# Kernel optimization log

Measured on AMD Instinct MI355X. Metric: run time of the kernel, lower is better.

## Reference

```python
import jax, jax.numpy as jnp
import numpy as np
from jax import lax

EPS = 1e-5
F_CH = 32  # TIM future channels = int(256/8)
B_CH = 32  # TIM past channels (note: source bug -> these are zeroed, not shifted)


def inorm(x):
    # InstanceNorm3d (no affine): normalize each (b, c) over (T, H, W), biased var
    m = jnp.mean(x, axis=(2, 3, 4), keepdims=True)
    v = jnp.var(x, axis=(2, 3, 4), keepdims=True)
    return (x - m) * lax.rsqrt(v + EPS)


def conv1x1(x, w):
    # pointwise conv: x [B,C,T,H,W], w [O,C]
    return jnp.einsum('bcthw,oc->bothw', x, w)


def dwconv(x, w, pad):
    # depthwise 3D conv; w [C,1,kd,kh,kw], pad = [(pd,pd),(ph,ph),(pw,pw)]
    return lax.conv_general_dilated(
        x, w, window_strides=(1, 1, 1), padding=pad,
        feature_group_count=x.shape[1],
        dimension_numbers=('NCDHW', 'OIDHW', 'NCDHW'))


def tim(x):
    # Non-circular temporal interlacing. Faithful to source (past slice is a no-op):
    # channels [0:f]  <- x shifted from future (t+1), zero-padded at last frame
    # channels [f:f+b] <- zeros
    # channels [f+b:] <- identity
    f, b = F_CH, B_CH
    fut = jnp.concatenate([x[:, :f, 1:], jnp.zeros_like(x[:, :f, :1])], axis=2)
    mid = jnp.zeros_like(x[:, f:f + b])
    return jnp.concatenate([fut, mid, x[:, f + b:]], axis=1)


def setup_inputs() -> dict:
    key = jax.random.key(0)
    ks = jax.random.split(key, 7)
    cin, hid, cout = 64, 256, 64
    x = jax.random.normal(ks[0], (4, cin, 16, 64, 64), dtype=jnp.float32)
    w1 = jax.random.normal(ks[1], (hid, cin), dtype=jnp.float32) * 0.05
    w_dw_s = jax.random.normal(ks[2], (hid, 1, 1, 3, 3), dtype=jnp.float32) * 0.1
    w_dw_t = jax.random.normal(ks[3], (hid, 1, 3, 1, 1), dtype=jnp.float32) * 0.1
    w_se1 = jax.random.normal(ks[4], (hid // 4, hid), dtype=jnp.float32) * 0.05
    w_se2 = jax.random.normal(ks[5], (hid, hid // 4), dtype=jnp.float32) * 0.05
    w_proj = jax.random.normal(ks[6], (cout, hid), dtype=jnp.float32) * 0.05
    return {'x': x, 'w1': w1, 'w_dw_s': w_dw_s, 'w_dw_t': w_dw_t,
            'w_se1': w_se1, 'w_se2': w_se2, 'w_proj': w_proj}


def reference(x, w1, w_dw_s, w_dw_t, w_se1, w_se2, w_proj):
    shortcut = x
    # stage1: expand 1x1 conv + IN + ReLU
    h = jax.nn.relu(inorm(conv1x1(x, w1)))
    # temporal interlace (zero-FLOP channel shift)
    h = tim(h)
    # stage2: depthwise spatial (1,3,3) + IN + ReLU
    h = jax.nn.relu(inorm(dwconv(h, w_dw_s, [(0, 0), (1, 1), (1, 1)])))
    # stage3: depthwise temporal (3,1,1) + IN + ReLU
    h = jax.nn.relu(inorm(dwconv(h, w_dw_t, [(1, 1), (0, 0), (0, 0)])))
    # squeeze-excite
    y = jnp.mean(h, axis=(2, 3, 4), keepdims=True)           # [B,C,1,1,1]
    y = jax.nn.relu(jnp.einsum('bcthw,oc->bothw', y, w_se1))
    y = jax.nn.sigmoid(jnp.einsum('bcthw,oc->bothw', y, w_se2))
    h = h * y
    # proj 1x1 + IN, residual, maxpool (1,2,2)
    out = inorm(conv1x1(h, w_proj)) + shortcut
    out = lax.reduce_window(out, -jnp.inf, lax.max,
                            (1, 1, 1, 2, 2), (1, 1, 1, 2, 2), 'VALID')
    return out
```

## Files before the change

kernel.cpp:

```cpp
#include <hip/hip_runtime.h>
#include <hip/hip_bf16.h>

#define B_   4
#define CIN  64
#define HID  256
#define COUT 64
#define T_   16
#define H_   64
#define W_   64
#define HW_  (H_*W_)
#define THW  (T_*HW_)
#define EPS  1e-5f

typedef unsigned short ushort_t;
typedef unsigned int   uint_t;
typedef short bf16x8 __attribute__((ext_vector_type(8)));
typedef float f32x4  __attribute__((ext_vector_type(4)));

#define SM3   4096
#define SIS3  5120
#define SSES  6144
#define SAL   7168
#define SBE   8192
__device__ float g_stats[10240];
__device__ float g_eps [4*1024*256];
__device__ float g_epss[4*1024*256];
__device__ ushort_t g_wpack[32768];

__device__ __forceinline__ float bf2f(ushort_t u) {
    return __uint_as_float(((uint_t)u) << 16);
}
__device__ __forceinline__ ushort_t f2bf(float f) {
    uint_t u = __float_as_uint(f);
    uint_t r = u + 0x7fffu + ((u >> 16) & 1u);
    return (ushort_t)(r >> 16);
}
__device__ __forceinline__ void loadnorm8(const ushort_t* p, float a, float bb,
                                          float* v) {
    uint4 u = *(const uint4*)p;
    uint_t uu[4] = {u.x, u.y, u.z, u.w};
    #pragma unroll
    for (int j = 0; j < 4; ++j) {
        v[2*j]   = fmaxf(fmaf(__uint_as_float(uu[j] << 16),         a, bb), 0.f);
        v[2*j+1] = fmaxf(fmaf(__uint_as_float(uu[j] & 0xffff0000u), a, bb), 0.f);
    }
}
__device__ __forceinline__ void loadnorm4(const ushort_t* p, float a, float bb,
                                          float* v) {
    uint2 u = *(const uint2*)p;
    uint_t uu[2] = {u.x, u.y};
    #pragma unroll
    for (int j = 0; j < 2; ++j) {
        v[2*j]   = fmaxf(fmaf(__uint_as_float(uu[j] << 16),         a, bb), 0.f);
        v[2*j+1] = fmaxf(fmaf(__uint_as_float(uu[j] & 0xffff0000u), a, bb), 0.f);
    }
}
__device__ __forceinline__ void unpacknorm2(uint2 k, float a, float bb, float* v) {
    uint_t uu[2] = {k.x, k.y};
    #pragma unroll
    for (int j = 0; j < 2; ++j) {
        v[2*j]   = fmaxf(fmaf(__uint_as_float(uu[j] << 16),         a, bb), 0.f);
        v[2*j+1] = fmaxf(fmaf(__uint_as_float(uu[j] & 0xffff0000u), a, bb), 0.f);
    }
}

__global__ __launch_bounds__(256) void k_prep(const float* __restrict__ w1,
                                              const float* __restrict__ wproj) {
    int idx = blockIdx.x*256 + threadIdx.x;
    {
        int j = idx & 7, lane = (idx>>3) & 63, ot = (idx>>9) & 3;
        int ks = (idx>>11) & 1, wv = idx >> 12;
        int ln = lane & 15, q = lane >> 4;
        int o = wv*64 + ot*16 + ln, k = ks*32 + q*8 + j;
        g_wpack[idx] = f2bf(w1[o*CIN + k]);
    }
    {
        int j = idx & 7, lane = (idx>>3) & 63, ot = (idx>>9) & 3, kg = idx >> 11;
        int ln = lane & 15, q = lane >> 4;
        int o = ot*16 + ln, k = kg*32 + q*8 + j;
        g_wpack[16384 + idx] = f2bf(wproj[o*HID + k]);
    }
}

__global__ __launch_bounds__(256) void k_expand(const float* __restrict__ x,
                                                ushort_t* __restrict__ h1, int b0) {
    union SMem {
        ushort_t Bs[64*72];
        float    red[2][256][16];
    };
    __shared__ SMem sm;
    const int tid = threadIdx.x;
    const int bb  = blockIdx.y, gb = b0 + bb;
    const int pos0 = blockIdx.x * 64;
    const int lane = tid & 63, wv = tid >> 6;
    const int q = lane >> 4, ln = lane & 15;

    bf16x8 af[2][4];
    #pragma unroll
    for (int ks = 0; ks < 2; ++ks)
        #pragma unroll
        for (int ot = 0; ot < 4; ++ot)
            af[ks][ot] = *(const bf16x8*)&g_wpack[(((wv*2+ks)*4+ot)<<9) + lane*8];

    #pragma unroll
    for (int i = 0; i < 4; ++i) {
        int lin = i*1024 + tid*4;
        int k = lin >> 6, n0 = lin & 63;
        float4 v = *(const float4*)&x[(size_t)(gb*CIN + k) * THW + pos0 + n0];
        ushort_t* d = &sm.Bs[k*72 + ((n0 + 16*((k>>3)&3)) & 63)];
        d[0] = f2bf(v.x); d[1] = f2bf(v.y); d[2] = f2bf(v.z); d[3] = f2bf(v.w);
    }
    __syncthreads();

    f32x4 acc[4][4];
    #pragma unroll
    for (int i = 0; i < 4; ++i)
        #pragma unroll
        for (int j = 0; j < 4; ++j)
            acc[i][j] = (f32x4){0.f,0.f,0.f,0.f};

    #pragma unroll
    for (int ks = 0; ks < 2; ++ks) {
        bf16x8 bfr[4];
        #pragma unroll
        for (int nt = 0; nt < 4; ++nt) {
            union { short s[8]; bf16x8 v; } bu;
            #pragma unroll
            for (int j = 0; j < 8; ++j) {
                int k = ks*32 + q*8 + j;
                int nn = (nt*16 + ln + 16*((k>>3)&3)) & 63;
                bu.s[j] = (short)sm.Bs[k*72 + nn];
            }
            bfr[nt] = bu.v;
        }
        #pragma unroll
        for (int ot = 0; ot < 4; ++ot)
            #pragma unroll
            for (int nt = 0; nt < 4; ++nt)
                acc[ot][nt] = __builtin_amdgcn_mfma_f32_16x16x32_bf16(
                    af[ks][ot], bfr[nt], acc[ot][nt], 0, 0, 0);
    }

    float sp_[16], ssp_[16];
    #pragma unroll
    for (int i = 0; i < 16; ++i) { sp_[i] = 0.f; ssp_[i] = 0.f; }

    #pragma unroll
    for (int ot = 0; ot < 4; ++ot)
        #pragma unroll
        for (int nt = 0; nt < 4; ++nt)
            #pragma unroll
            for (int r = 0; r < 4; ++r) {
                float vv = acc[ot][nt][r];
                int o = wv*64 + ot*16 + q*4 + r;
                int n = nt*16 + ln;
                h1[((size_t)bb*HID + o)*THW + pos0 + n] = f2bf(vv);
                sp_[ot*4+r] += vv;
                ssp_[ot*4+r] = fmaf(vv, vv, ssp_[ot*4+r]);
            }

    __syncthreads();
    #pragma unroll
    for (int i = 0; i < 16; ++i) {
        int o = wv*64 + (i>>2)*16 + q*4 + (i&3);
        sm.red[0][o][ln] = sp_[i];
        sm.red[1][o][ln] = ssp_[i];
    }
    __syncthreads();
    {
        float s = 0.f, ss = 0.f;
        #pragma unroll
        for (int l = 0; l < 16; ++l) {
            s  += sm.red[0][tid][l];
            ss += sm.red[1][tid][l];
        }
        size_t base = ((size_t)bb*1024 + blockIdx.x)*256 + tid;
        g_eps [base] = s;
        g_epss[base] = ss;
    }
}

__global__ __launch_bounds__(1024) void k_mid(const ushort_t* __restrict__ h1,
                                              const float* __restrict__ wdws,
                                              const float* __restrict__ wdwt,
                                              ushort_t* __restrict__ h3) {
    const int tid = threadIdx.x;
    const int bc  = blockIdx.x;
    const int o   = bc & (HID-1);
    const int bb  = bc >> 8;
    const int wid = tid >> 6, lane = tid & 63;

    if (o >= 32 && o < 64) {
        if (tid == 0) {
            g_stats[SM3  + bc] = 0.f;
            g_stats[SIS3 + bc] = 1.f / sqrtf(EPS);
            g_stats[SSES + bc] = 0.f;
        }
        return;
    }

    __shared__ float pl[2][64*65];
    __shared__ float ls[16], lss[16];
    __shared__ float sa, sb;

    {
        const float* ps  = &g_eps [((size_t)bb*1024)*256 + o];
        const float* pss = &g_epss[((size_t)bb*1024)*256 + o];
        float s  = ps [(size_t)tid*256];
        float ss = pss[(size_t)tid*256];
        #pragma unroll
        for (int m = 32; m > 0; m >>= 1) {
            s  += __shfl_xor(s,  m);
            ss += __shfl_xor(ss, m);
        }
        if (lane == 0) { ls[wid] = s; lss[wid] = ss; }
        __syncthreads();
        if (tid == 0) {
            float st = 0.f, sst = 0.f;
            #pragma unroll
            for (int i = 0; i < 16; ++i) { st += ls[i]; sst += lss[i]; }
            float m = st * (1.f/THW);
            float v = sst * (1.f/THW) - m*m;
            float is = 1.f / sqrtf(v + EPS);
            sa = is; sb = -m * is;
        }
        __syncthreads();
    }
    const float a1 = sa, b1 = sb;

    const int fut = (o < 32) ? 1 : 0;
    const int y   = tid >> 4;
    const int x0  = (tid & 15) * 4;
    const ushort_t* chp = h1 + (size_t)bc * THW;

    float wf[9];
    #pragma unroll
    for (int k = 0; k < 9; ++k) wf[k] = wdws[o*9 + k];

    {
        const ushort_t* sp = chp + (size_t)(fut ? 1 : 0) * HW_ + tid*4;
        float v[4];
        loadnorm4(sp, a1, b1, v);
        float* dst = &pl[0][y*65 + x0];
        #pragma unroll
        for (int i = 0; i < 4; ++i) dst[i] = v[i];
    }
    __syncthreads();

    uint2 keep[16];
    float s2 = 0.f, ss2 = 0.f;
    const int lastp = fut ? (T_-2) : (T_-1);

    #pragma unroll
    for (int t = 0; t < T_; ++t) {
        if (t < lastp) {
            int np = t + 1;
            const ushort_t* sp = chp + (size_t)(fut ? np+1 : np)*HW_ + tid*4;
            float v[4];
            loadnorm4(sp, a1, b1, v);
            float* dst = &pl[np & 1][y*65 + x0];
            #pragma unroll
            for (int i = 0; i < 4; ++i) dst[i] = v[i];
        }
        if (fut && t == T_-1) {
            keep[t] = (uint2){0u, 0u};
        } else {
            const float* plane = pl[t & 1];
            float v[3][6];
            #pragma unroll
            for (int dy = 0; dy < 3; ++dy) {
                int yy = y + dy - 1;
                if (yy < 0 || yy >= H_) {
                    #pragma unroll
                    for (int j = 0; j < 6; ++j) v[dy][j] = 0.f;
                } else {
                    const float* rp = &plane[yy*65];
                    v[dy][0] = (x0 == 0)  ? 0.f : rp[x0-1];
                    #pragma unroll
                    for (int i = 0; i < 4; ++i) v[dy][1+i] = rp[x0+i];
                    v[dy][5] = (x0 == 60) ? 0.f : rp[x0+4];
                }
            }
            uint_t outp[2];
            #pragma unroll
            for (int i2 = 0; i2 < 2; ++i2) {
                float o0 = 0.f, o1 = 0.f;
                #pragma unroll
                for (int dy = 0; dy < 3; ++dy)
                    #pragma unroll
                    for (int dx = 0; dx < 3; ++dx) {
                        float w = wf[dy*3+dx];
                        o0 = fmaf(w, v[dy][2*i2 + dx],     o0);
                        o1 = fmaf(w, v[dy][2*i2 + 1 + dx], o1);
                    }
                ushort_t u0 = f2bf(o0), u1 = f2bf(o1);
                float r0 = bf2f(u0), r1 = bf2f(u1);
                s2 += r0 + r1; ss2 = fmaf(r0, r0, fmaf(r1, r1, ss2));
                outp[i2] = (uint_t)u0 | ((uint_t)u1 << 16);
            }
            keep[t].x = outp[0]; keep[t].y = outp[1];
        }
        __syncthreads();
    }

    {
        float s = s2, ss = ss2;
        #pragma unroll
        for (int m = 32; m > 0; m >>= 1) {
            s  += __shfl_xor(s,  m);
            ss += __shfl_xor(ss, m);
        }
        if (lane == 0) { ls[wid] = s; lss[wid] = ss; }
        __syncthreads();
        if (tid == 0) {
            float st = 0.f, sst = 0.f;
            #pragma unroll
            for (int i = 0; i < 16; ++i) { st += ls[i]; sst += lss[i]; }
            float m = st * (1.f/THW);
            float v = sst * (1.f/THW) - m*m;
            float is = 1.f / sqrtf(v + EPS);
            sa = is; sb = -m * is;
        }
        __syncthreads();
    }
    const float a2 = sa, b2 = sb;

    const float w0 = wdwt[o*3+0], w1 = wdwt[o*3+1], w2 = wdwt[o*3+2];
    ushort_t* op = h3 + (size_t)bc * THW + tid*4;

    float p[4], c[4], n[4];
    #pragma unroll
    for (int i = 0; i < 4; ++i) p[i] = 0.f;
    unpacknorm2(keep[0], a2, b2, c);
    unpacknorm2(keep[1], a2, b2, n);

    float s3 = 0.f, ss3 = 0.f;
    #pragma unroll
    for (int t = 0; t < T_; ++t) {
        uint_t outp[2];
        #pragma unroll
        for (int i2 = 0; i2 < 2; ++i2) {
            float o0 = fmaf(w0, p[2*i2],   fmaf(w1, c[2*i2],   w2 * n[2*i2]));
            float o1 = fmaf(w0, p[2*i2+1], fmaf(w1, c[2*i2+1], w2 * n[2*i2+1]));
            ushort_t u0 = f2bf(o0), u1 = f2bf(o1);
            float r0 = bf2f(u0), r1 = bf2f(u1);
            s3 += r0 + r1; ss3 = fmaf(r0, r0, fmaf(r1, r1, ss3));
            outp[i2] = (uint_t)u0 | ((uint_t)u1 << 16);
        }
        uint2 r; r.x = outp[0]; r.y = outp[1];
        *(uint2*)(op + (size_t)t*HW_) = r;

        #pragma unroll
        for (int i = 0; i < 4; ++i) { p[i] = c[i]; c[i] = n[i]; }
        if (t + 2 < T_) unpacknorm2(keep[t+2], a2, b2, n);
        else {
            #pragma unroll
            for (int i = 0; i < 4; ++i) n[i] = 0.f;
        }
        keep[t] = r;
    }

    {
        float s = s3, ss = ss3;
        #pragma unroll
        for (int m = 32; m > 0; m >>= 1) {
            s  += __shfl_xor(s,  m);
            ss += __shfl_xor(ss, m);
        }
        if (lane == 0) { ls[wid] = s; lss[wid] = ss; }
        __syncthreads();
        if (tid == 0) {
            float st = 0.f, sst = 0.f;
            #pragma unroll
            for (int i = 0; i < 16; ++i) { st += ls[i]; sst += lss[i]; }
            float m = st * (1.f/THW);
            float v = sst * (1.f/THW) - m*m;
            float is = 1.f / sqrtf(v + EPS);
            g_stats[SM3  + bc] = m;
            g_stats[SIS3 + bc] = is;
            sa = is; sb = -m * is;
        }
        __syncthreads();
    }

    const float a3 = sa, b3 = sb;
    float sse = 0.f;
    #pragma unroll
    for (int t = 0; t < T_; ++t) {
        uint_t uu[2] = {keep[t].x, keep[t].y};
        #pragma unroll
        for (int j = 0; j < 2; ++j) {
            sse += fmaxf(fmaf(__uint_as_float(uu[j] << 16),         a3, b3), 0.f);
            sse += fmaxf(fmaf(__uint_as_float(uu[j] & 0xffff0000u), a3, b3), 0.f);
        }
    }
    #pragma unroll
    for (int m = 32; m > 0; m >>= 1) sse += __shfl_xor(sse, m);
    if (lane == 0) ls[wid] = sse;
    __syncthreads();
    if (tid == 0) {
        float st = 0.f;
        #pragma unroll
        for (int i = 0; i < 16; ++i) st += ls[i];
        g_stats[SSES + bc] = st * (1.f/THW);
    }
}

__global__ __launch_bounds__(256) void k_semlp(const float* __restrict__ wse1,
                                               const float* __restrict__ wse2) {
    __shared__ float mv[HID];
    __shared__ float y1[64];
    const int bb = blockIdx.x, tid = threadIdx.x;
    mv[tid] = g_stats[SSES + bb*HID + tid];
    __syncthreads();
    if (tid < 64) {
        float acc = 0.f;
        #pragma unroll 8
        for (int c = 0; c < HID; ++c) acc = fmaf(wse1[tid*HID + c], mv[c], acc);
        y1[tid] = fmaxf(acc, 0.f);
    }
    __syncthreads();
    float z = 0.f;
    #pragma unroll
    for (int c = 0; c < 64; ++c) z = fmaf(wse2[tid*64 + c], y1[c], z);
    float se = 1.f / (1.f + expf(-z));
    const int bc = bb*HID + tid;
    float al = g_stats[SIS3 + bc] * se;
    if (tid >= 32 && tid < 64) al = 0.f;
    g_stats[SAL + bc] = al;
    g_stats[SBE + bc] = -g_stats[SM3 + bc] * al;
}

__global__ __launch_bounds__(256) void k_proj(const ushort_t* __restrict__ h3,
                                              float* __restrict__ proj) {
    __shared__ ushort_t Bs[64*136];
    const int tid = threadIdx.x;
    const int bb  = blockIdx.y;
    const int pos0 = blockIdx.x * 128;
    const int lane = tid & 63, wv = tid >> 6;
    const int q = lane >> 4, ln = lane & 15;

    f32x4 acc[4][2];
    #pragma unroll
    for (int i = 0; i < 4; ++i) {
        acc[i][0] = (f32x4){0.f,0.f,0.f,0.f};
        acc[i][1] = (f32x4){0.f,0.f,0.f,0.f};
    }

    for (int kc = 0; kc < 4; ++kc) {
        #pragma unroll
        for (int i = 0; i < 8; ++i) {
            int lin = i*1024 + tid*4;
            int kl = lin >> 7, n0 = lin & 127;
            int ch = bb*HID + kc*64 + kl;
            float al = g_stats[SAL + ch], be = g_stats[SBE + ch];
            ushort_t* d = &Bs[kl*136 + ((n0 + 16*((kl>>3)&7)) & 127)];
            if (al == 0.f) {
                d[0] = 0; d[1] = 0; d[2] = 0; d[3] = 0;
            } else {
                uint2 u = *(const uint2*)&h3[(size_t)ch * THW + pos0 + n0];
                float f0 = __uint_as_float(u.x << 16);
                float f1 = __uint_as_float(u.x & 0xffff0000u);
                float f2 = __uint_as_float(u.y << 16);
                float f3 = __uint_as_float(u.y & 0xffff0000u);
                d[0] = f2bf(fmaxf(fmaf(f0, al, be), 0.f));
                d[1] = f2bf(fmaxf(fmaf(f1, al, be), 0.f));
                d[2] = f2bf(fmaxf(fmaf(f2, al, be), 0.f));
                d[3] = f2bf(fmaxf(fmaf(f3, al, be), 0.f));
            }
        }
        __syncthreads();

        #pragma unroll
        for (int ks = 0; ks < 2; ++ks) {
            int kg = kc*2 + ks;
            bf16x8 af[4];
            #pragma unroll
            for (int ot = 0; ot < 4; ++ot)
                af[ot] = *(const bf16x8*)&g_wpack[16384 + ((kg*4+ot)<<9) + lane*8];
            bf16x8 bfr[2];
            #pragma unroll
            for (int nt = 0; nt < 2; ++nt) {
                union { short s[8]; bf16x8 v; } bu;
                #pragma unroll
                for (int j = 0; j < 8; ++j) {
                    int kl = ks*32 + q*8 + j;
                    int nn = (wv*32 + nt*16 + ln + 16*((kl>>3)&7)) & 127;
                    bu.s[j] = (short)Bs[kl*136 + nn];
                }
                bfr[nt] = bu.v;
            }
            #pragma unroll
            for (int ot = 0; ot < 4; ++ot)
                #pragma unroll
                for (int nt = 0; nt < 2; ++nt)
                    acc[ot][nt] = __builtin_amdgcn_mfma_f32_16x16x32_bf16(
                        af[ot], bfr[nt], acc[ot][nt], 0, 0, 0);
        }
        __syncthreads();
    }

    #pragma unroll
    for (int ot = 0; ot < 4; ++ot)
        #pragma unroll
        for (int nt = 0; nt < 2; ++nt)
            #pragma unroll
            for (int r = 0; r < 4; ++r) {
                int o = ot*16 + q*4 + r;
                int n = wv*32 + nt*16 + ln;
                proj[((size_t)bb*COUT + o)*THW + pos0 + n] = acc[ot][nt][r];
            }
}

__global__ __launch_bounds__(1024) void k_final(const float* __restrict__ proj,
                                                const float* __restrict__ x,
                                                float* __restrict__ out, int b0) {
    const int bo  = blockIdx.x;
    const int tid = threadIdx.x;
    const float* p = proj + (size_t)bo * THW;

    float s = 0.f, ss = 0.f;
    #pragma unroll
    for (int i = 0; i < THW/(1024*4); ++i) {
        float4 u = *(const float4*)(p + i*4096 + tid*4);
        s += u.x; ss = fmaf(u.x, u.x, ss);
        s += u.y; ss = fmaf(u.y, u.y, ss);
        s += u.z; ss = fmaf(u.z, u.z, ss);
        s += u.w; ss = fmaf(u.w, u.w, ss);
    }
    #pragma unroll
    for (int off = 32; off > 0; off >>= 1) {
        s  += __shfl_down(s,  off, 64);
        ss += __shfl_down(ss, off, 64);
    }
    __shared__ float ls[16], lss[16];
    __shared__ float sa, sb;
    int wid = tid >> 6, lane = tid & 63;
    if (lane == 0) { ls[wid] = s; lss[wid] = ss; }
    __syncthreads();
    if (tid == 0) {
        float st = 0.f, sst = 0.f;
        #pragma unroll
        for (int i = 0; i < 16; ++i) { st += ls[i]; sst += lss[i]; }
        float m = st * (1.f/THW);
        float v = sst * (1.f/THW) - m*m;
        float is = 1.f / sqrtf(v + EPS);
        sa = is; sb = -m * is;
    }
    __syncthreads();
    const float a = sa, bb = sb;

    const size_t gbase = (size_t)(b0*COUT + bo) * THW;
    float* op = out + (size_t)(b0*COUT + bo) * (T_*1024);
    #pragma unroll
    for (int i = 0; i < 16; ++i) {
        int idx = i*1024 + tid;
        int xx = idx & 31, yy = (idx >> 5) & 31, t = idx >> 10;
        float m = -3.4e38f;
        #pragma unroll
        for (int r = 0; r < 2; ++r) {
            size_t off = (size_t)t*HW_ + (size_t)(2*yy + r)*W_ + 2*xx;
            float2 p2 = *(const float2*)(p + off);
            float2 x2 = *(const float2*)(x + gbase + off);
            float v0 = fmaf(p2.x, a, bb) + x2.x;
            float v1 = fmaf(p2.y, a, bb) + x2.y;
            m = fmaxf(m, fmaxf(v0, v1));
        }
        op[idx] = m;
    }
}

extern "C" void kernel_launch(void* const* d_in, const int* in_sizes, int n_in,
                              void* d_out, int out_size, void* d_ws, size_t ws_size,
                              hipStream_t stream) {
    const float* x     = (const float*)d_in[0];
    const float* w1    = (const float*)d_in[1];
    const float* wdws  = (const float*)d_in[2];
    const float* wdwt  = (const float*)d_in[3];
    const float* wse1  = (const float*)d_in[4];
    const float* wse2  = (const float*)d_in[5];
    const float* wproj = (const float*)d_in[6];
    float* out = (float*)d_out;

    const size_t perb = 2ull * HID * THW * sizeof(ushort_t);
    int nb = (ws_size >= 4*perb) ? 4 : (ws_size >= 2*perb) ? 2 : 1;

    k_prep<<<64, 256, 0, stream>>>(w1, wproj);

    for (int b0 = 0; b0 < B_; b0 += nb) {
        char* ws = (char*)d_ws;
        ushort_t* h1   = (ushort_t*)ws;
        ushort_t* h3   = h1;
        float*    proj = (float*)(ws + (size_t)nb * HID*THW*2);

        k_expand<<<dim3(THW/64, nb), 256, 0, stream>>>(x, h1, b0);
        k_mid   <<<nb*HID, 1024, 0, stream>>>(h1, wdws, wdwt, h3);
        k_semlp <<<nb, 256, 0, stream>>>(wse1, wse2);
        k_proj  <<<dim3(THW/128, nb), 256, 0, stream>>>(h3, proj);
        k_final <<<nb*COUT, 1024, 0, stream>>>(proj, x, out, b0);
    }
}
```

Baseline: 367.5 us.

## Fuse projection stats into k_proj, pad mid-stage planes, prefetch input rows

k_proj now reduces per-block sum and sum-of-squares of its accumulators and writes partials, so k_final no longer rereads the whole fp32 projection tensor just to compute InstanceNorm statistics. The per-channel stat partials are transposed to be contiguous, which makes the reads in k_mid coalesced. k_mid uses a zero-padded 66x67 shared plane to drop boundary branches, register-prefetches the next-next plane, and sets a launch-bounds occupancy hint. The costs are extra reduction work and a barrier in k_proj, plus register pressure from the occupancy hint.

```diff
diff --git a/kernel.cpp b/kernel.cpp
--- a/kernel.cpp
+++ b/kernel.cpp
@@ -23,8 +23,10 @@
 #define SAL   7168
 #define SBE   8192
 __device__ float g_stats[10240];
-__device__ float g_eps [4*1024*256];
-__device__ float g_epss[4*1024*256];
+__device__ float g_eps [4*256*1024];
+__device__ float g_epss[4*256*1024];
+__device__ float g_pps [4*64*512];
+__device__ float g_ppss[4*64*512];
 __device__ ushort_t g_wpack[32768];
 
 __device__ __forceinline__ float bf2f(ushort_t u) {
@@ -34,26 +36,6 @@
     uint_t u = __float_as_uint(f);
     uint_t r = u + 0x7fffu + ((u >> 16) & 1u);
     return (ushort_t)(r >> 16);
-}
-__device__ __forceinline__ void loadnorm8(const ushort_t* p, float a, float bb,
-                                          float* v) {
-    uint4 u = *(const uint4*)p;
-    uint_t uu[4] = {u.x, u.y, u.z, u.w};
-    #pragma unroll
-    for (int j = 0; j < 4; ++j) {
-        v[2*j]   = fmaxf(fmaf(__uint_as_float(uu[j] << 16),         a, bb), 0.f);
-        v[2*j+1] = fmaxf(fmaf(__uint_as_float(uu[j] & 0xffff0000u), a, bb), 0.f);
-    }
-}
-__device__ __forceinline__ void loadnorm4(const ushort_t* p, float a, float bb,
-                                          float* v) {
-    uint2 u = *(const uint2*)p;
-    uint_t uu[2] = {u.x, u.y};
-    #pragma unroll
-    for (int j = 0; j < 2; ++j) {
-        v[2*j]   = fmaxf(fmaf(__uint_as_float(uu[j] << 16),         a, bb), 0.f);
-        v[2*j+1] = fmaxf(fmaf(__uint_as_float(uu[j] & 0xffff0000u), a, bb), 0.f);
-    }
 }
 __device__ __forceinline__ void unpacknorm2(uint2 k, float a, float bb, float* v) {
     uint_t uu[2] = {k.x, k.y};
@@ -174,16 +156,16 @@
             s  += sm.red[0][tid][l];
             ss += sm.red[1][tid][l];
         }
-        size_t base = ((size_t)bb*1024 + blockIdx.x)*256 + tid;
+        size_t base = ((size_t)bb*256 + tid)*1024 + blockIdx.x;
         g_eps [base] = s;
         g_epss[base] = ss;
     }
 }
 
-__global__ __launch_bounds__(1024) void k_mid(const ushort_t* __restrict__ h1,
-                                              const float* __restrict__ wdws,
-                                              const float* __restrict__ wdwt,
-                                              ushort_t* __restrict__ h3) {
+__global__ __launch_bounds__(1024, 8) void k_mid(const ushort_t* __restrict__ h1,
+                                                 const float* __restrict__ wdws,
+                                                 const float* __restrict__ wdwt,
+                                                 ushort_t* __restrict__ h3) {
     const int tid = threadIdx.x;
     const int bc  = blockIdx.x;
     const int o   = bc & (HID-1);
@@ -199,21 +181,30 @@
         return;
     }
 
-    __shared__ float pl[2][64*65];
+    __shared__ float pl[2][66*67];
     __shared__ float ls[16], lss[16];
     __shared__ float sa, sb;
 
     {
-        const float* ps  = &g_eps [((size_t)bb*1024)*256 + o];
-        const float* pss = &g_epss[((size_t)bb*1024)*256 + o];
-        float s  = ps [(size_t)tid*256];
-        float ss = pss[(size_t)tid*256];
+        const float* ps  = &g_eps [((size_t)bb*256 + o)*1024];
+        const float* pss = &g_epss[((size_t)bb*256 + o)*1024];
+        float s  = ps [tid];
+        float ss = pss[tid];
         #pragma unroll
         for (int m = 32; m > 0; m >>= 1) {
             s  += __shfl_xor(s,  m);
             ss += __shfl_xor(ss, m);
         }
         if (lane == 0) { ls[wid] = s; lss[wid] = ss; }
+        if (tid < 66) {
+            #pragma unroll
+            for (int b = 0; b < 2; ++b) {
+                pl[b][tid]         = 0.f;
+                pl[b][65*67 + tid] = 0.f;
+                pl[b][tid*67]      = 0.f;
+                pl[b][tid*67 + 65] = 0.f;
+            }
+        }
         __syncthreads();
         if (tid == 0) {
             float st = 0.f, sst = 0.f;
@@ -232,35 +223,37 @@
     const int y   = tid >> 4;
     const int x0  = (tid & 15) * 4;
     const ushort_t* chp = h1 + (size_t)bc * THW;
+    const int lastp = fut ? (T_-2) : (T_-1);
 
     float wf[9];
     #pragma unroll
     for (int k = 0; k < 9; ++k) wf[k] = wdws[o*9 + k];
 
+    uint2 sreg[2];
+    sreg[0] = *(const uint2*)(chp + (size_t)fut*HW_ + tid*4);
     {
-        const ushort_t* sp = chp + (size_t)(fut ? 1 : 0) * HW_ + tid*4;
-        float v[4];
-        loadnorm4(sp, a1, b1, v);
-        float* dst = &pl[0][y*65 + x0];
-        #pragma unroll
-        for (int i = 0; i < 4; ++i) dst[i] = v[i];
-    }
+        float vv[4];
+        unpacknorm2(sreg[0], a1, b1, vv);
+        float* dst = &pl[0][(y+1)*67 + x0 + 1];
+        #pragma unroll
+        for (int i = 0; i < 4; ++i) dst[i] = vv[i];
+    }
+    sreg[1] = *(const uint2*)(chp + (size_t)(1+fut)*HW_ + tid*4);
     __syncthreads();
 
     uint2 keep[16];
     float s2 = 0.f, ss2 = 0.f;
-    const int lastp = fut ? (T_-2) : (T_-1);
 
     #pragma unroll
     for (int t = 0; t < T_; ++t) {
-        if (t < lastp) {
-            int np = t + 1;
-            const ushort_t* sp = chp + (size_t)(fut ? np+1 : np)*HW_ + tid*4;
-            float v[4];
-            loadnorm4(sp, a1, b1, v);
-            float* dst = &pl[np & 1][y*65 + x0];
-            #pragma unroll
-            for (int i = 0; i < 4; ++i) dst[i] = v[i];
+        if (t + 2 <= lastp)
+            sreg[t & 1] = *(const uint2*)(chp + (size_t)(t+2+fut)*HW_ + tid*4);
+        if (t + 1 <= lastp) {
+            float vv[4];
+            unpacknorm2(sreg[(t+1) & 1], a1, b1, vv);
+            float* dst = &pl[(t+1) & 1][(y+1)*67 + x0 + 1];
+            #pragma unroll
+            for (int i = 0; i < 4; ++i) dst[i] = vv[i];
         }
         if (fut && t == T_-1) {
             keep[t] = (uint2){0u, 0u};
@@ -269,17 +262,9 @@
             float v[3][6];
             #pragma unroll
             for (int dy = 0; dy < 3; ++dy) {
-                int yy = y + dy - 1;
-                if (yy < 0 || yy >= H_) {
-                    #pragma unroll
-                    for (int j = 0; j < 6; ++j) v[dy][j] = 0.f;
-                } else {
-                    const float* rp = &plane[yy*65];
-                    v[dy][0] = (x0 == 0)  ? 0.f : rp[x0-1];
-                    #pragma unroll
-                    for (int i = 0; i < 4; ++i) v[dy][1+i] = rp[x0+i];
-                    v[dy][5] = (x0 == 60) ? 0.f : rp[x0+4];
-                }
+                const float* rp = &plane[(y + dy)*67 + x0];
+                #pragma unroll
+                for (int j = 0; j < 6; ++j) v[dy][j] = rp[j];
             }
             uint_t outp[2];
             #pragma unroll
@@ -434,6 +419,7 @@
 __global__ __launch_bounds__(256) void k_proj(const ushort_t* __restrict__ h3,
                                               float* __restrict__ proj) {
     __shared__ ushort_t Bs[64*136];
+    __shared__ float rs[64][4], rss[64][4];
     const int tid = threadIdx.x;
     const int bb  = blockIdx.y;
     const int pos0 = blockIdx.x * 128;
@@ -510,6 +496,33 @@
                 int n = wv*32 + nt*16 + ln;
                 proj[((size_t)bb*COUT + o)*THW + pos0 + n] = acc[ot][nt][r];
             }
+
+    #pragma unroll
+    for (int ot = 0; ot < 4; ++ot)
+        #pragma unroll
+        for (int r = 0; r < 4; ++r) {
+            float s  = acc[ot][0][r] + acc[ot][1][r];
+            float ss = fmaf(acc[ot][0][r], acc[ot][0][r],
+                            acc[ot][1][r] * acc[ot][1][r]);
+            #pragma unroll
+            for (int m = 1; m < 16; m <<= 1) {
+                s  += __shfl_xor(s,  m);
+                ss += __shfl_xor(ss, m);
+            }
+            if (ln == 0) {
+                int o = ot*16 + q*4 + r;
+                rs[o][wv]  = s;
+                rss[o][wv] = ss;
+            }
+        }
+    __syncthreads();
+    if (tid < 64) {
+        float s  = rs[tid][0]  + rs[tid][1]  + rs[tid][2]  + rs[tid][3];
+        float ss = rss[tid][0] + rss[tid][1] + rss[tid][2] + rss[tid][3];
+        size_t base = ((size_t)bb*64 + tid)*512 + blockIdx.x;
+        g_pps [base] = s;
+        g_ppss[base] = ss;
+    }
 }
 
 __global__ __launch_bounds__(1024) void k_final(const float* __restrict__ proj,
@@ -520,13 +533,9 @@
     const float* p = proj + (size_t)bo * THW;
 
     float s = 0.f, ss = 0.f;
-    #pragma unroll
-    for (int i = 0; i < THW/(1024*4); ++i) {
-        float4 u = *(const float4*)(p + i*4096 + tid*4);
-        s += u.x; ss = fmaf(u.x, u.x, ss);
-        s += u.y; ss = fmaf(u.y, u.y, ss);
-        s += u.z; ss = fmaf(u.z, u.z, ss);
-        s += u.w; ss = fmaf(u.w, u.w, ss);
+    if (tid < 512) {
+        s  = g_pps [(size_t)bo*512 + tid];
+        ss = g_ppss[(size_t)bo*512 + tid];
     }
     #pragma unroll
     for (int off = 32; off > 0; off >>= 1) {
```

New measurement: 454.9 us. +23.8%, slower.
